# Optimization experiments

Measured on AMD Instinct MI355X. Metric: run time of the kernel, lower is better.

Reference implementation:

```python
import jax, jax.numpy as jnp
import numpy as np

N = 100000   # nodes
E = 1600000  # edges
C = 128      # hidden_channels
L = 3        # num_layers
V = 128      # embedding vocab


def setup_inputs() -> dict:
    key = jax.random.key(0)
    ks = jax.random.split(key, 10)
    s = 1.0 / np.sqrt(C)
    return {
        "x_idx": jax.random.randint(ks[0], (N,), 0, V),
        "edge_index": jax.random.randint(ks[1], (2, E), 0, N),
        "edge_weight": jax.random.uniform(ks[2], (E,), dtype=jnp.float32),
        "emb": jax.random.normal(ks[3], (V, C), dtype=jnp.float32),
        "conv_w": jax.random.uniform(ks[4], (L, C, C), minval=-s, maxval=s, dtype=jnp.float32),
        "conv_b": jnp.zeros((L, C), dtype=jnp.float32),
        "lin1_w": jax.random.uniform(ks[5], (C, C), minval=-s, maxval=s, dtype=jnp.float32),
        "lin1_b": jnp.zeros((C,), dtype=jnp.float32),
        "lin2_w": jax.random.uniform(ks[6], (C, 2), minval=-s, maxval=s, dtype=jnp.float32),
        "lin2_b": jnp.zeros((2,), dtype=jnp.float32),
    }


def reference(x_idx, edge_index, edge_weight, emb, conv_w, conv_b,
              lin1_w, lin1_b, lin2_w, lin2_b):
    # GCNConv (PyG): add self-loops (weight 1), symmetric normalization
    row, col = edge_index[0], edge_index[1]
    loop = jnp.arange(N)
    r = jnp.concatenate([row, loop])
    c = jnp.concatenate([col, loop])
    w = jnp.concatenate([edge_weight, jnp.ones((N,), edge_weight.dtype)])
    deg = jax.ops.segment_sum(w, c, num_segments=N)            # [N]
    dinv = jnp.where(deg > 0, jax.lax.rsqrt(deg), 0.0)
    norm = dinv[r] * w * dinv[c]                               # [E+N]

    x = emb[x_idx]                                             # [N, C]
    for i in range(L):
        xw = x @ conv_w[i]                                     # [N, C]
        # message: norm * xw[src], aggregate at dst
        x = jax.ops.segment_sum(norm[:, None] * xw[r], c, num_segments=N) + conv_b[i]
        if i < L - 1:
            x = jax.nn.relu(x)  # dropout is identity in eval mode

    x = jax.nn.relu(x @ lin1_w + lin1_b)
    return x @ lin2_w + lin2_b                                 # [N, 2]
```

## Files before the change

### kernel.cpp

```cpp
#include <hip/hip_runtime.h>
#include <hip/hip_fp16.h>

#define NN 100000
#define NE 1600000
#define CC 128
#define NBIN 782
#define BPW 128
#define MAXB 2560
#define NHB 256
#define EPB 6250

typedef _Float16 f16x8 __attribute__((ext_vector_type(8)));
typedef float    f32x4 __attribute__((ext_vector_type(4)));

__global__ __launch_bounds__(256) void k_hist(const int* __restrict__ ei,
                                              int* __restrict__ hist) {
    __shared__ int h[NBIN];
    for (int i = threadIdx.x; i < NBIN; i += 256) h[i] = 0;
    __syncthreads();
    int base = blockIdx.x * EPB;
    for (int i = threadIdx.x; i < EPB; i += 256) {
        int d = ei[NE + base + i];
        atomicAdd(&h[d >> 7], 1);
    }
    __syncthreads();
    for (int i = threadIdx.x; i < NBIN; i += 256)
        hist[blockIdx.x * NBIN + i] = h[i];
}

__global__ __launch_bounds__(256) void k_scanA(const int* __restrict__ hist,
                                               int* __restrict__ blockBase,
                                               int* __restrict__ binTotal) {
    __shared__ int s[256];
    int bin = blockIdx.x, t = threadIdx.x;
    int v = hist[t * NBIN + bin];
    s[t] = v; __syncthreads();
    for (int off = 1; off < 256; off <<= 1) {
        int x = (t >= off) ? s[t - off] : 0;
        __syncthreads();
        s[t] += x;
        __syncthreads();
    }
    blockBase[t * NBIN + bin] = s[t] - v;
    if (t == 255) binTotal[bin] = s[255];
}

__global__ __launch_bounds__(1024) void k_scanB(const int* __restrict__ binTotal,
                                                int* __restrict__ binStart) {
    __shared__ int s[1024];
    int t = threadIdx.x;
    int v = (t < NBIN) ? binTotal[t] : 0;
    s[t] = v; __syncthreads();
    for (int off = 1; off < 1024; off <<= 1) {
        int x = (t >= off) ? s[t - off] : 0;
        __syncthreads();
        s[t] += x;
        __syncthreads();
    }
    if (t < NBIN) binStart[t] = s[t] - v;
    if (t == 1023) binStart[NBIN] = s[1023];
}

__global__ __launch_bounds__(256) void k_pass2(const int* __restrict__ ei,
                                               const float* __restrict__ ew,
                                               const int* __restrict__ binStart,
                                               const int* __restrict__ blockBase,
                                               int2* __restrict__ pay,
                                               unsigned char* __restrict__ key) {
    __shared__ int cur[NBIN];
    int blk = blockIdx.x;
    for (int i = threadIdx.x; i < NBIN; i += 256)
        cur[i] = binStart[i] + blockBase[blk * NBIN + i];
    __syncthreads();
    int base = blk * EPB;
    for (int i = threadIdx.x; i < EPB; i += 256) {
        int e = base + i;
        int d = ei[NE + e];
        int src = ei[e];
        float w = ew[e];
        int pos = atomicAdd(&cur[d >> 7], 1);
        pay[pos] = make_int2(src, __float_as_int(w));
        key[pos] = (unsigned char)(d & 127);
    }
}

__global__ __launch_bounds__(256) void k_pass3(const int* __restrict__ binStart,
                                               const int2* __restrict__ pay,
                                               const unsigned char* __restrict__ key,
                                               int2* __restrict__ csr,
                                               int* __restrict__ rowptr,
                                               float* __restrict__ dinv) {
    __shared__ int2 sp[MAXB];
    __shared__ unsigned char sk[MAXB];
    __shared__ int hist[BPW], excl[BPW], cur[BPW];
    __shared__ float degw[BPW];
    int b = blockIdx.x, t = threadIdx.x;
    int s0 = binStart[b], s1 = binStart[b + 1];
    int n = s1 - s0;
    if (t < BPW) { hist[t] = 0; degw[t] = 0.f; }
    __syncthreads();
    for (int i = t; i < n; i += 256) {
        int2 p = pay[s0 + i];
        unsigned char k = key[s0 + i];
        sp[i] = p; sk[i] = k;
        atomicAdd(&hist[k], 1);
    }
    __syncthreads();
    if (t < BPW) excl[t] = hist[t];
    __syncthreads();
    for (int off = 1; off < BPW; off <<= 1) {
        int x = (t < BPW && t >= off) ? excl[t - off] : 0;
        __syncthreads();
        if (t < BPW) excl[t] += x;
        __syncthreads();
    }
    if (t < BPW) {
        int ex = excl[t] - hist[t];
        excl[t] = ex;
        cur[t] = ex;
    }
    __syncthreads();
    int node0 = b * BPW;
    if (t < BPW && node0 + t < NN) rowptr[node0 + t] = s0 + excl[t];
    if (b == NBIN - 1 && t == 0) rowptr[NN] = NE;
    for (int i = t; i < n; i += 256) {
        int2 p = sp[i];
        unsigned char k = sk[i];
        int pos = atomicAdd(&cur[k], 1);
        csr[s0 + pos] = p;
        atomicAdd(&degw[k], __int_as_float(p.y));
    }
    __syncthreads();
    if (t < BPW && node0 + t < NN) dinv[node0 + t] = rsqrtf(1.f + degw[t]);
}

__global__ void k_mkcsr0(const int2* __restrict__ csr, const int* __restrict__ xidx,
                         const float* __restrict__ dinv, int2* __restrict__ csr0) {
    int e = blockIdx.x * 256 + threadIdx.x;
    if (e < NE) {
        int2 c = csr[e];
        csr0[e] = make_int2(xidx[c.x],
                            __float_as_int(__int_as_float(c.y) * dinv[c.x]));
    }
}

__global__ void k_wcvt(const float* __restrict__ conv_w, const float* __restrict__ lin1_w,
                       _Float16* __restrict__ wt) {
    int t = blockIdx.x * 256 + threadIdx.x;
    int l = t >> 14, r = t & 16383;
    int j = r >> 7, k = r & 127;
    const float* src = (l < 2) ? (conv_w + (l + 1) * 16384) : lin1_w;
    wt[l * 16384 + j * 128 + k] = (_Float16)src[k * 128 + j];
}

__global__ void k_embw(const float* __restrict__ emb, const float* __restrict__ w0,
                       __half2* __restrict__ ewh) {
    int t = blockIdx.x * 256 + threadIdx.x;
    int i = t >> 6, jp = t & 63;
    int j0 = jp * 2;
    float a0 = 0.f, a1 = 0.f;
    for (int k = 0; k < 128; k++) {
        float e = emb[i * 128 + k];
        a0 = fmaf(e, w0[k * 128 + j0], a0);
        a1 = fmaf(e, w0[k * 128 + j0 + 1], a1);
    }
    ewh[t] = __floats2half2_rn(a0, a1);
}

template <int SELF_TABLE, int RELU>
__device__ __forceinline__ void agg_core(const _Float16* __restrict__ src16,
                                         const int2* __restrict__ csr,
                                         const int* __restrict__ rowptr,
                                         const int* __restrict__ xidx,
                                         const float* __restrict__ dinv,
                                         const float* __restrict__ bias,
                                         _Float16* __restrict__ xout) {
    int wave = threadIdx.x >> 6, lane = threadIdx.x & 63;
    int g = lane >> 4, sub = lane & 15;
    int v = blockIdx.x * 4 + wave;
    if (v >= NN) return;
    int beg = rowptr[v], end = rowptr[v + 1];
    float acc[8];
#pragma unroll
    for (int i = 0; i < 8; i++) acc[i] = 0.f;
    int e = beg;
    while (e + 8 <= end) {
        int2 c0 = csr[e + g];
        int2 c1 = csr[e + 4 + g];
        f16x8 t0 = *reinterpret_cast<const f16x8*>(&src16[(size_t)c0.x * 128 + sub * 8]);
        f16x8 t1 = *reinterpret_cast<const f16x8*>(&src16[(size_t)c1.x * 128 + sub * 8]);
        float w0 = __int_as_float(c0.y), w1 = __int_as_float(c1.y);
#pragma unroll
        for (int i = 0; i < 8; i++) acc[i] = fmaf(w0, (float)t0[i], acc[i]);
#pragma unroll
        for (int i = 0; i < 8; i++) acc[i] = fmaf(w1, (float)t1[i], acc[i]);
        e += 8;
    }
    for (; e < end; e += 4) {
        int idx = e + g;
        bool ok = idx < end;
        int2 c0 = csr[ok ? idx : beg];
        float w0 = ok ? __int_as_float(c0.y) : 0.f;
        f16x8 t0 = *reinterpret_cast<const f16x8*>(&src16[(size_t)c0.x * 128 + sub * 8]);
#pragma unroll
        for (int i = 0; i < 8; i++) acc[i] = fmaf(w0, (float)t0[i], acc[i]);
    }
#pragma unroll
    for (int i = 0; i < 8; i++) {
        acc[i] += __shfl_down(acc[i], 32);
        acc[i] += __shfl_down(acc[i], 16);
    }
    if (g == 0) {
        float dv = dinv[v];
        size_t selfoff = SELF_TABLE ? (size_t)xidx[v] * 128 : (size_t)v * 128;
        f16x8 sf = *reinterpret_cast<const f16x8*>(&src16[selfoff + sub * 8]);
        float4 b0 = reinterpret_cast<const float4*>(bias)[sub * 2];
        float4 b1 = reinterpret_cast<const float4*>(bias)[sub * 2 + 1];
        float bb[8] = {b0.x, b0.y, b0.z, b0.w, b1.x, b1.y, b1.z, b1.w};
        f16x8 o;
#pragma unroll
        for (int i = 0; i < 8; i++) {
            float self = SELF_TABLE ? dv * (float)sf[i] : (float)sf[i];
            float r = fmaf(dv, acc[i] + self, bb[i]);
            if (RELU) r = fmaxf(r, 0.f);
            o[i] = (_Float16)r;
        }
        *reinterpret_cast<f16x8*>(&xout[(size_t)v * 128 + sub * 8]) = o;
    }
}

__global__ void k_agg0(const int2* __restrict__ csr0, const int* __restrict__ rowptr,
                       const int* __restrict__ xidx, const float* __restrict__ dinv,
                       const _Float16* __restrict__ ewh, const float* __restrict__ bias,
                       _Float16* __restrict__ xout) {
    agg_core<1, 1>(ewh, csr0, rowptr, xidx, dinv, bias, xout);
}

__global__ void k_agg_r(const _Float16* __restrict__ y, const int* __restrict__ rowptr,
                        const int2* __restrict__ csr, const float* __restrict__ dinv,
                        const float* __restrict__ bias, _Float16* __restrict__ xout) {
    agg_core<0, 1>(y, csr, rowptr, nullptr, dinv, bias, xout);
}

__global__ void k_agg_n(const _Float16* __restrict__ y, const int* __restrict__ rowptr,
                        const int2* __restrict__ csr, const float* __restrict__ dinv,
                        const float* __restrict__ bias, _Float16* __restrict__ xout) {
    agg_core<0, 0>(y, csr, rowptr, nullptr, dinv, bias, xout);
}

template <int MODE>
__global__ __launch_bounds__(256) void k_mgemm(const _Float16* __restrict__ A,
                                               const _Float16* __restrict__ Wt,
                                               const float* __restrict__ dinv,
                                               const float* __restrict__ bias,
                                               _Float16* __restrict__ yout,
                                               const float* __restrict__ w2,
                                               const float* __restrict__ b2,
                                               float* __restrict__ outf) {
    int wid = threadIdx.x >> 6, lane = threadIdx.x & 63;
    int lc = lane & 15, lg = lane >> 4;
    int arow = blockIdx.x * 64 + wid * 16 + lc;
    bool rok = arow < NN;

    f32x4 acc[8];
#pragma unroll
    for (int j = 0; j < 8; j++) acc[j] = (f32x4){0.f, 0.f, 0.f, 0.f};

#pragma unroll
    for (int kc = 0; kc < 4; kc++) {
        int k0 = kc * 32 + lg * 8;
        f16x8 a = {0, 0, 0, 0, 0, 0, 0, 0};
        if (rok) a = *reinterpret_cast<const f16x8*>(&A[arow * 128 + k0]);
#pragma unroll
        for (int j = 0; j < 8; j++) {
            f16x8 b = *reinterpret_cast<const f16x8*>(&Wt[(j * 16 + lc) * 128 + k0]);
            acc[j] = __builtin_amdgcn_mfma_f32_16x16x32_f16(a, b, acc[j], 0, 0, 0);
        }
    }

    int orow0 = blockIdx.x * 64 + wid * 16 + lg * 4;
    if (MODE == 0) {
        float dv[4];
#pragma unroll
        for (int r = 0; r < 4; r++)
            dv[r] = (orow0 + r < NN) ? dinv[orow0 + r] : 0.f;
#pragma unroll
        for (int j = 0; j < 8; j++) {
#pragma unroll
            for (int r = 0; r < 4; r++) {
                int orow = orow0 + r;
                if (orow < NN)
                    yout[orow * 128 + j * 16 + lc] = (_Float16)(dv[r] * acc[j][r]);
            }
        }
    } else {
        float bj[8], w0j[8], w1j[8];
#pragma unroll
        for (int j = 0; j < 8; j++) {
            int c = j * 16 + lc;
            bj[j] = bias[c];
            w0j[j] = w2[c * 2 + 0];
            w1j[j] = w2[c * 2 + 1];
        }
        float bb0 = b2[0], bb1 = b2[1];
#pragma unroll
        for (int r = 0; r < 4; r++) {
            float p0 = 0.f, p1 = 0.f;
#pragma unroll
            for (int j = 0; j < 8; j++) {
                float h = fmaxf(acc[j][r] + bj[j], 0.f);
                p0 = fmaf(h, w0j[j], p0);
                p1 = fmaf(h, w1j[j], p1);
            }
#pragma unroll
            for (int m = 1; m < 16; m <<= 1) {
                p0 += __shfl_xor(p0, m);
                p1 += __shfl_xor(p1, m);
            }
            int orow = orow0 + r;
            if (lc == 0 && orow < NN)
                *reinterpret_cast<float2*>(&outf[orow * 2]) =
                    make_float2(p0 + bb0, p1 + bb1);
        }
    }
}

extern "C" void kernel_launch(void* const* d_in, const int* in_sizes, int n_in,
                              void* d_out, int out_size, void* d_ws, size_t ws_size,
                              hipStream_t stream) {
    const int*   x_idx  = (const int*)d_in[0];
    const int*   ei     = (const int*)d_in[1];
    const float* ew     = (const float*)d_in[2];
    const float* emb    = (const float*)d_in[3];
    const float* conv_w = (const float*)d_in[4];
    const float* conv_b = (const float*)d_in[5];
    const float* lin1_w = (const float*)d_in[6];
    const float* lin1_b = (const float*)d_in[7];
    const float* lin2_w = (const float*)d_in[8];
    const float* lin2_b = (const float*)d_in[9];
    float* out = (float*)d_out;

    char* ws = (char*)d_ws;
    size_t off = 0;
    auto alloc = [&](size_t bytes) -> void* {
        void* p = ws + off;
        off += (bytes + 255) & ~(size_t)255;
        return p;
    };
    float*         dinv      = (float*)alloc(NN * 4);
    int*           rowptr    = (int*)alloc((NN + 1) * 4);
    int*           hist      = (int*)alloc((size_t)NHB * NBIN * 4);
    int*           blockBase = (int*)alloc((size_t)NHB * NBIN * 4);
    int*           binTotal  = (int*)alloc(NBIN * 4);
    int*           binStart  = (int*)alloc((NBIN + 1) * 4);
    int2*          pay       = (int2*)alloc((size_t)NE * 8);
    unsigned char* key       = (unsigned char*)alloc(NE);
    int2*          csr       = (int2*)alloc((size_t)NE * 8);
    int2*          csr0      = (int2*)alloc((size_t)NE * 8);
    _Float16*      ewh       = (_Float16*)alloc(128 * 128 * 2);
    _Float16*      wt        = (_Float16*)alloc(3 * 128 * 128 * 2);
    _Float16*      xbuf      = (_Float16*)alloc((size_t)NN * CC * 2);
    _Float16*      ybuf      = (_Float16*)alloc((size_t)NN * CC * 2);
    (void)ws_size;

    const int NBe = (NE + 255) / 256;
    const int NBg = (NN + 63) / 64;

    k_hist<<<NHB, 256, 0, stream>>>(ei, hist);
    k_scanA<<<NBIN, 256, 0, stream>>>(hist, blockBase, binTotal);
    k_scanB<<<1, 1024, 0, stream>>>(binTotal, binStart);
    k_pass2<<<NHB, 256, 0, stream>>>(ei, ew, binStart, blockBase, pay, key);
    k_pass3<<<NBIN, 256, 0, stream>>>(binStart, pay, key, csr, rowptr, dinv);
    k_mkcsr0<<<NBe, 256, 0, stream>>>(csr, x_idx, dinv, csr0);
    k_wcvt<<<192, 256, 0, stream>>>(conv_w, lin1_w, wt);

    k_embw<<<32, 256, 0, stream>>>(emb, conv_w, (__half2*)ewh);
    k_agg0<<<NN / 4, 256, 0, stream>>>(csr0, rowptr, x_idx, dinv, ewh,
                                       conv_b + 0 * CC, xbuf);
    k_mgemm<0><<<NBg, 256, 0, stream>>>(xbuf, wt + 0 * 16384, dinv, nullptr, ybuf,
                                        nullptr, nullptr, nullptr);
    k_agg_r<<<NN / 4, 256, 0, stream>>>(ybuf, rowptr, csr, dinv, conv_b + 1 * CC, xbuf);
    k_mgemm<0><<<NBg, 256, 0, stream>>>(xbuf, wt + 1 * 16384, dinv, nullptr, ybuf,
                                        nullptr, nullptr, nullptr);
    k_agg_n<<<NN / 4, 256, 0, stream>>>(ybuf, rowptr, csr, dinv, conv_b + 2 * CC, xbuf);
    k_mgemm<1><<<NBg, 256, 0, stream>>>(xbuf, wt + 2 * 16384, dinv, lin1_b, nullptr,
                                        lin2_w, lin2_b, out);
}
```

Before: 390.6 us.

## Fuse prep kernels, merge scans via last-block pattern, software-pipeline aggregation gathers

Merges the histogram, weight conversion and embedding-weight precompute into one launch. The two scan kernels become one, with the last-finishing block (tracked by an atomic counter) doing the bin-level scan. The aggregation loop now prefetches three 4-edge batches ahead, so gathers are in flight while FMAs run. It also uses nontemporal loads for the CSR and nontemporal stores for outputs. Together these cut launch overhead and expose more memory-level parallelism, at the cost of extra clamped loads past each row's end and more registers.

```diff
diff --git a/kernel.cpp b/kernel.cpp
--- a/kernel.cpp
+++ b/kernel.cpp
@@ -13,25 +13,54 @@
 typedef _Float16 f16x8 __attribute__((ext_vector_type(8)));
 typedef float    f32x4 __attribute__((ext_vector_type(4)));
 
-__global__ __launch_bounds__(256) void k_hist(const int* __restrict__ ei,
-                                              int* __restrict__ hist) {
-    __shared__ int h[NBIN];
-    for (int i = threadIdx.x; i < NBIN; i += 256) h[i] = 0;
-    __syncthreads();
-    int base = blockIdx.x * EPB;
-    for (int i = threadIdx.x; i < EPB; i += 256) {
-        int d = ei[NE + base + i];
-        atomicAdd(&h[d >> 7], 1);
-    }
-    __syncthreads();
-    for (int i = threadIdx.x; i < NBIN; i += 256)
-        hist[blockIdx.x * NBIN + i] = h[i];
+__global__ __launch_bounds__(256) void k_prep0(const int* __restrict__ ei,
+                                               const float* __restrict__ conv_w,
+                                               const float* __restrict__ lin1_w,
+                                               const float* __restrict__ emb,
+                                               int* __restrict__ hist,
+                                               _Float16* __restrict__ wt,
+                                               __half2* __restrict__ ewh,
+                                               int* __restrict__ counter) {
+    int blk = blockIdx.x;
+    if (blk < NHB) {
+        __shared__ int h[NBIN];
+        for (int i = threadIdx.x; i < NBIN; i += 256) h[i] = 0;
+        __syncthreads();
+        int base = blk * EPB;
+        for (int i = threadIdx.x; i < EPB; i += 256) {
+            int d = ei[NE + base + i];
+            atomicAdd(&h[d >> 7], 1);
+        }
+        __syncthreads();
+        for (int i = threadIdx.x; i < NBIN; i += 256)
+            hist[blk * NBIN + i] = h[i];
+        if (blk == 0 && threadIdx.x == 0) *counter = 0;
+    } else if (blk < NHB + 192) {
+        int t = (blk - NHB) * 256 + threadIdx.x;
+        int l = t >> 14, r = t & 16383;
+        int j = r >> 7, k = r & 127;
+        const float* src = (l < 2) ? (conv_w + (l + 1) * 16384) : lin1_w;
+        wt[l * 16384 + j * 128 + k] = (_Float16)src[k * 128 + j];
+    } else {
+        int t = (blk - NHB - 192) * 256 + threadIdx.x;
+        int i = t >> 6, jp = t & 63, j0 = jp * 2;
+        float a0 = 0.f, a1 = 0.f;
+        for (int k = 0; k < 128; k++) {
+            float e = emb[i * 128 + k];
+            a0 = fmaf(e, conv_w[k * 128 + j0], a0);
+            a1 = fmaf(e, conv_w[k * 128 + j0 + 1], a1);
+        }
+        ewh[t] = __floats2half2_rn(a0, a1);
+    }
 }
 
 __global__ __launch_bounds__(256) void k_scanA(const int* __restrict__ hist,
                                                int* __restrict__ blockBase,
-                                               int* __restrict__ binTotal) {
+                                               int* __restrict__ binTotal,
+                                               int* __restrict__ binStart,
+                                               int* __restrict__ counter) {
     __shared__ int s[256];
+    __shared__ bool amLast;
     int bin = blockIdx.x, t = threadIdx.x;
     int v = hist[t * NBIN + bin];
     s[t] = v; __syncthreads();
@@ -42,23 +71,37 @@
         __syncthreads();
     }
     blockBase[t * NBIN + bin] = s[t] - v;
-    if (t == 255) binTotal[bin] = s[255];
-}
-
-__global__ __launch_bounds__(1024) void k_scanB(const int* __restrict__ binTotal,
-                                                int* __restrict__ binStart) {
-    __shared__ int s[1024];
-    int t = threadIdx.x;
-    int v = (t < NBIN) ? binTotal[t] : 0;
-    s[t] = v; __syncthreads();
-    for (int off = 1; off < 1024; off <<= 1) {
+    if (t == 255) {
+        binTotal[bin] = s[255];
+        __threadfence();
+        int d = atomicAdd(counter, 1);
+        amLast = (d == NBIN - 1);
+    }
+    __syncthreads();
+    if (!amLast) return;
+    int vals[4], loc[4];
+    int sum = 0;
+#pragma unroll
+    for (int j = 0; j < 4; j++) {
+        int idx = t * 4 + j;
+        int x = (idx < NBIN) ? atomicAdd(&binTotal[idx], 0) : 0;
+        loc[j] = sum; sum += x; vals[j] = x;
+    }
+    __syncthreads();
+    s[t] = sum; __syncthreads();
+    for (int off = 1; off < 256; off <<= 1) {
         int x = (t >= off) ? s[t - off] : 0;
         __syncthreads();
         s[t] += x;
         __syncthreads();
     }
-    if (t < NBIN) binStart[t] = s[t] - v;
-    if (t == 1023) binStart[NBIN] = s[1023];
+    int base = s[t] - sum;
+#pragma unroll
+    for (int j = 0; j < 4; j++) {
+        int idx = t * 4 + j;
+        if (idx < NBIN) binStart[idx] = base + loc[j];
+    }
+    if (t == 255) binStart[NBIN] = s[255];
 }
 
 __global__ __launch_bounds__(256) void k_pass2(const int* __restrict__ ei,
@@ -144,29 +187,6 @@
     }
 }
 
-__global__ void k_wcvt(const float* __restrict__ conv_w, const float* __restrict__ lin1_w,
-                       _Float16* __restrict__ wt) {
-    int t = blockIdx.x * 256 + threadIdx.x;
-    int l = t >> 14, r = t & 16383;
-    int j = r >> 7, k = r & 127;
-    const float* src = (l < 2) ? (conv_w + (l + 1) * 16384) : lin1_w;
-    wt[l * 16384 + j * 128 + k] = (_Float16)src[k * 128 + j];
-}
-
-__global__ void k_embw(const float* __restrict__ emb, const float* __restrict__ w0,
-                       __half2* __restrict__ ewh) {
-    int t = blockIdx.x * 256 + threadIdx.x;
-    int i = t >> 6, jp = t & 63;
-    int j0 = jp * 2;
-    float a0 = 0.f, a1 = 0.f;
-    for (int k = 0; k < 128; k++) {
-        float e = emb[i * 128 + k];
-        a0 = fmaf(e, w0[k * 128 + j0], a0);
-        a1 = fmaf(e, w0[k * 128 + j0 + 1], a1);
-    }
-    ewh[t] = __floats2half2_rn(a0, a1);
-}
-
 template <int SELF_TABLE, int RELU>
 __device__ __forceinline__ void agg_core(const _Float16* __restrict__ src16,
                                          const int2* __restrict__ csr,
@@ -180,31 +200,37 @@
     int v = blockIdx.x * 4 + wave;
     if (v >= NN) return;
     int beg = rowptr[v], end = rowptr[v + 1];
+    int nb = (end - beg + 3) >> 2;
+    int cl = max(end - 1, 0);
+    const unsigned long long* csr64 =
+        reinterpret_cast<const unsigned long long*>(csr);
+
+    auto ld = [&](int b, float& w) -> const f16x8* {
+        int idx = beg + b * 4 + g;
+        int idxc = idx < end ? idx : cl;
+        unsigned long long raw = __builtin_nontemporal_load(csr64 + idxc);
+        int s = (int)(unsigned)(raw & 0xffffffffu);
+        w = (idx < end) ? __int_as_float((int)(raw >> 32)) : 0.f;
+        return reinterpret_cast<const f16x8*>(&src16[(size_t)s * 128 + sub * 8]);
+    };
+
+    float w0, w1, w2, w3;
+    f16x8 t0 = *ld(0, w0);
+    f16x8 t1 = *ld(1, w1);
+    f16x8 t2 = *ld(2, w2);
+
     float acc[8];
 #pragma unroll
     for (int i = 0; i < 8; i++) acc[i] = 0.f;
-    int e = beg;
-    while (e + 8 <= end) {
-        int2 c0 = csr[e + g];
-        int2 c1 = csr[e + 4 + g];
-        f16x8 t0 = *reinterpret_cast<const f16x8*>(&src16[(size_t)c0.x * 128 + sub * 8]);
-        f16x8 t1 = *reinterpret_cast<const f16x8*>(&src16[(size_t)c1.x * 128 + sub * 8]);
-        float w0 = __int_as_float(c0.y), w1 = __int_as_float(c1.y);
+
+    for (int b = 0; b < nb; b++) {
+        f16x8 t3 = *ld(b + 3, w3);
 #pragma unroll
         for (int i = 0; i < 8; i++) acc[i] = fmaf(w0, (float)t0[i], acc[i]);
-#pragma unroll
-        for (int i = 0; i < 8; i++) acc[i] = fmaf(w1, (float)t1[i], acc[i]);
-        e += 8;
-    }
-    for (; e < end; e += 4) {
-        int idx = e + g;
-        bool ok = idx < end;
-        int2 c0 = csr[ok ? idx : beg];
-        float w0 = ok ? __int_as_float(c0.y) : 0.f;
-        f16x8 t0 = *reinterpret_cast<const f16x8*>(&src16[(size_t)c0.x * 128 + sub * 8]);
-#pragma unroll
-        for (int i = 0; i < 8; i++) acc[i] = fmaf(w0, (float)t0[i], acc[i]);
-    }
+        w0 = w1; w1 = w2; w2 = w3;
+        t0 = t1; t1 = t2; t2 = t3;
+    }
+
 #pragma unroll
     for (int i = 0; i < 8; i++) {
         acc[i] += __shfl_down(acc[i], 32);
@@ -225,7 +251,8 @@
             if (RELU) r = fmaxf(r, 0.f);
             o[i] = (_Float16)r;
         }
-        *reinterpret_cast<f16x8*>(&xout[(size_t)v * 128 + sub * 8]) = o;
+        __builtin_nontemporal_store(
+            o, reinterpret_cast<f16x8*>(&xout[(size_t)v * 128 + sub * 8]));
     }
 }
 
@@ -353,6 +380,7 @@
     int*           blockBase = (int*)alloc((size_t)NHB * NBIN * 4);
     int*           binTotal  = (int*)alloc(NBIN * 4);
     int*           binStart  = (int*)alloc((NBIN + 1) * 4);
+    int*           counter   = (int*)alloc(256);
     int2*          pay       = (int2*)alloc((size_t)NE * 8);
     unsigned char* key       = (unsigned char*)alloc(NE);
     int2*          csr       = (int2*)alloc((size_t)NE * 8);
@@ -366,15 +394,13 @@
     const int NBe = (NE + 255) / 256;
     const int NBg = (NN + 63) / 64;
 
-    k_hist<<<NHB, 256, 0, stream>>>(ei, hist);
-    k_scanA<<<NBIN, 256, 0, stream>>>(hist, blockBase, binTotal);
-    k_scanB<<<1, 1024, 0, stream>>>(binTotal, binStart);
+    k_prep0<<<NHB + 192 + 32, 256, 0, stream>>>(ei, conv_w, lin1_w, emb,
+                                                hist, wt, (__half2*)ewh, counter);
+    k_scanA<<<NBIN, 256, 0, stream>>>(hist, blockBase, binTotal, binStart, counter);
     k_pass2<<<NHB, 256, 0, stream>>>(ei, ew, binStart, blockBase, pay, key);
     k_pass3<<<NBIN, 256, 0, stream>>>(binStart, pay, key, csr, rowptr, dinv);
     k_mkcsr0<<<NBe, 256, 0, stream>>>(csr, x_idx, dinv, csr0);
-    k_wcvt<<<192, 256, 0, stream>>>(conv_w, lin1_w, wt);
-
-    k_embw<<<32, 256, 0, stream>>>(emb, conv_w, (__half2*)ewh);
+
     k_agg0<<<NN / 4, 256, 0, stream>>>(csr0, rowptr, x_idx, dinv, ewh,
                                        conv_b + 0 * CC, xbuf);
     k_mgemm<0><<<NBg, 256, 0, stream>>>(xbuf, wt + 0 * 16384, dinv, nullptr, ybuf,
```

New measurement: 444.1 us. 13.7% more time.
